# Optimization experiments

Measured on AMD Instinct MI355X. Metric: run time of the kernel, lower is better.

## Reference

```python
import jax, jax.numpy as jnp
import numpy as np

GRID = 4
N = GRID * GRID  # 16 nodes
CIN = 16
HID = 64
HEADS = 4
OUT = 256
NEG_SLOPE = 0.2  # PyG GATConv default leaky relu slope
LN_EPS = 1e-5


def _adj_mask():
    # 4-connected grid adjacency + self loops (PyG GATConv add_self_loops=True)
    m = np.zeros((N, N), dtype=bool)
    for i in range(GRID):
        for j in range(GRID):
            u = i * GRID + j
            if j + 1 < GRID:
                v = i * GRID + j + 1
                m[u, v] = m[v, u] = True
            if i + 1 < GRID:
                v = (i + 1) * GRID + j
                m[u, v] = m[v, u] = True
    np.fill_diagonal(m, True)
    return m

ADJ = jnp.asarray(_adj_mask())  # [N, N], adj[i, j] = j is a (self-)neighbor of i


def gat_layer(h, W, a_src, a_dst, b, concat):
    """PyG GATConv on the fixed grid graph, dense-masked form.
    h: [B, N, Fin]; W: [Fin, HEADS*C]; a_src/a_dst: [HEADS, C]."""
    B = h.shape[0]
    H, C = a_src.shape
    wh = (h @ W).reshape(B, N, H, C)                       # [B, N, H, C]
    e_src = jnp.einsum('bnhc,hc->bnh', wh, a_src)          # alpha_src . Wh_j
    e_dst = jnp.einsum('bnhc,hc->bnh', wh, a_dst)          # alpha_dst . Wh_i
    # score[b, i, j, h]: target i attends to source j
    e = e_dst[:, :, None, :] + e_src[:, None, :, :]
    e = jax.nn.leaky_relu(e, NEG_SLOPE)
    e = jnp.where(ADJ[None, :, :, None], e, -1e9)
    alpha = jax.nn.softmax(e, axis=2)                      # softmax over sources j
    out = jnp.einsum('bijh,bjhc->bihc', alpha, wh)         # [B, N, H, C]
    if concat:
        out = out.reshape(B, N, H * C)
    else:
        out = out.mean(axis=2)
    return out + b


def setup_inputs() -> dict:
    key = jax.random.key(0)
    ks = jax.random.split(key, 24)
    s = 0.05
    B = 16384
    inp = {
        'x': jax.random.normal(ks[0], (B, CIN, GRID, GRID), dtype=jnp.float32),
        'w_in': jax.random.normal(ks[1], (CIN, HID), dtype=jnp.float32) * s,
        'b_in': jnp.zeros((HID,), jnp.float32),
        # GAT layer 0: in 64 -> 4 heads x 64, concat
        'W0': jax.random.normal(ks[2], (HID, HEADS * HID), dtype=jnp.float32) * s,
        'asrc0': jax.random.normal(ks[3], (HEADS, HID), dtype=jnp.float32) * s,
        'adst0': jax.random.normal(ks[4], (HEADS, HID), dtype=jnp.float32) * s,
        'bb0': jnp.zeros((HEADS * HID,), jnp.float32),
        # GAT layer 1: in 256 -> 4 heads x 64, concat
        'W1': jax.random.normal(ks[5], (HEADS * HID, HEADS * HID), dtype=jnp.float32) * s,
        'asrc1': jax.random.normal(ks[6], (HEADS, HID), dtype=jnp.float32) * s,
        'adst1': jax.random.normal(ks[7], (HEADS, HID), dtype=jnp.float32) * s,
        'bb1': jnp.zeros((HEADS * HID,), jnp.float32),
        # GAT layer 2: in 256 -> 4 heads x 64, mean over heads (concat=False)
        'W2': jax.random.normal(ks[8], (HEADS * HID, HEADS * HID), dtype=jnp.float32) * s,
        'asrc2': jax.random.normal(ks[9], (HEADS, HID), dtype=jnp.float32) * s,
        'adst2': jax.random.normal(ks[10], (HEADS, HID), dtype=jnp.float32) * s,
        'bb2': jnp.zeros((HID,), jnp.float32),
        # output MLP: 64 -> 128 (LN, ReLU) -> 256
        'w1': jax.random.normal(ks[11], (HID, OUT // 2), dtype=jnp.float32) * s,
        'b1': jnp.zeros((OUT // 2,), jnp.float32),
        'ln_g': jnp.ones((OUT // 2,), jnp.float32),
        'ln_b': jnp.zeros((OUT // 2,), jnp.float32),
        'w2': jax.random.normal(ks[12], (OUT // 2, OUT), dtype=jnp.float32) * s,
        'b2': jnp.zeros((OUT,), jnp.float32),
    }
    return inp


def reference(x, w_in, b_in, W0, asrc0, adst0, bb0, W1, asrc1, adst1, bb1,
              W2, asrc2, adst2, bb2, w1, b1, ln_g, ln_b, w2, b2):
    B = x.shape[0]
    # grid_to_graph: (B, C, H, W) -> (B, N, C) node features
    h = jnp.transpose(x, (0, 2, 3, 1)).reshape(B, N, CIN)
    h = jax.nn.relu(h @ w_in + b_in)
    h = gat_layer(h, W0, asrc0, adst0, bb0, concat=True)
    h = jax.nn.relu(h)  # dropout is identity at inference
    h = gat_layer(h, W1, asrc1, adst1, bb1, concat=True)
    h = jax.nn.relu(h)
    h = gat_layer(h, W2, asrc2, adst2, bb2, concat=False)  # [B, N, 64]
    g = h.mean(axis=1)  # global_mean_pool over the 16 nodes of each graph
    # MLP with LayerNorm
    y = g @ w1 + b1
    mu = y.mean(axis=-1, keepdims=True)
    var = ((y - mu) ** 2).mean(axis=-1, keepdims=True)
    y = (y - mu) * jax.lax.rsqrt(var + LN_EPS) * ln_g + ln_b
    y = jax.nn.relu(y)
    return y @ w2 + b2
```

## Files before the change

### kernel.cpp

```cpp
#include <hip/hip_runtime.h>
#include <hip/hip_bf16.h>

typedef short s8v __attribute__((ext_vector_type(8)));
typedef short s4v __attribute__((ext_vector_type(4)));
typedef float f4v __attribute__((ext_vector_type(4)));

#define HSTR 264
#define WSTR 36
#define AP   18

__device__ constexpr unsigned KMASK[16] = {
  0x0013u,0x0027u,0x004Eu,0x008Cu,
  0x0131u,0x0272u,0x04E4u,0x08C8u,
  0x1310u,0x2720u,0x4E40u,0x8C80u,
  0x3100u,0x7200u,0xE400u,0xC800u};

__device__ __forceinline__ short f2b(float x){
  __hip_bfloat16 h = __float2bfloat16(x);
  return *reinterpret_cast<short*>(&h);
}
__device__ __forceinline__ float b2f(short s){
  __hip_bfloat16 h = *reinterpret_cast<__hip_bfloat16*>(&s);
  return __bfloat162float(h);
}

__global__ __launch_bounds__(256) void prep_all(
  const float* __restrict__ W0, const float* __restrict__ as0, const float* __restrict__ ad0,
  const float* __restrict__ W1, const float* __restrict__ as1, const float* __restrict__ ad1,
  const float* __restrict__ W2, const float* __restrict__ as2, const float* __restrict__ ad2,
  const float* __restrict__ w_in,
  short* __restrict__ ws)
{
  short* WPin = ws;
  short* WP0  = ws + 2048;
  short* WP1  = ws + 2048 + 17408;
  short* WP2  = ws + 2048 + 17408 + 69632;

  const int t = threadIdx.x, l = t & 63;
  const int gid = blockIdx.x*4 + (t >> 6);

  if (gid < 288){
    const float* W; short* WP; int u = gid, f, s, KS;
    if (u < 32)      { W = W0; WP = WP0; KS = 2; f = u >> 1; s = u & 1; }
    else if (u < 160){ u -= 32;  W = W1; WP = WP1; KS = 8; f = u >> 3; s = u & 7; }
    else             { u -= 160; W = W2; WP = WP2; KS = 8; f = u >> 3; s = u & 7; }
    const int lq = l & 15, quad = l >> 4;
    union { s8v v; short s16[8]; } o;
    #pragma unroll
    for (int j = 0; j < 8; ++j)
      o.s16[j] = f2b(W[(s*32 + quad*8 + j)*256 + f*16 + lq]);
    *(s8v*)(WP + ((f*KS + s)*64 + l)*8) = o.v;
  } else if (gid < 292){
    const int f = gid - 288;
    const int lq = l & 15, quad = l >> 4;
    union { s8v v; short s16[8]; } o;
    #pragma unroll
    for (int j = 0; j < 8; ++j){
      const int k = quad*8 + j;
      o.s16[j] = (k < 16) ? f2b(w_in[k*64 + f*16 + lq]) : (short)0;
    }
    *(s8v*)(WPin + (f*64 + l)*8) = o.v;
  } else {
    int u = gid - 292;
    const float* W; const float* as; const float* ad; short* WP; int KS, k;
    if (u < 64)      { W=W0; as=as0; ad=ad0; WP=WP0; KS=2; k=u; }
    else if (u < 320){ u-=64;  W=W1; as=as1; ad=ad1; WP=WP1; KS=8; k=u; }
    else             { u-=320; W=W2; as=as2; ad=ad2; WP=WP2; KS=8; k=u; }
    float v[8];
    #pragma unroll
    for (int h = 0; h < 4; ++h){
      const float wv_ = W[k*256 + h*64 + l];
      v[h]   = wv_ * as[h*64 + l];
      v[4+h] = wv_ * ad[h*64 + l];
    }
    #pragma unroll
    for (int s = 1; s < 64; s <<= 1)
      #pragma unroll
      for (int uu = 0; uu < 8; ++uu) v[uu] += __shfl_xor(v[uu], s, 64);
    if (l < 16){
      const float r = (l < 8) ? v[l] : 0.f;
      WP[((16*KS + (k >> 5))*64 + ((k >> 3) & 3)*16 + l)*8 + (k & 7)] = f2b(r);
    }
  }
}

template<int KS, bool MEAN>
__device__ __forceinline__ void gat_layer(short* bufH, short* whT, short* alphaS,
    const short* __restrict__ WP, const float* __restrict__ bbias,
    float* gsm, const int t)
{
  const int l = t & 63, wv = t >> 6, lq = l & 15, quad = l >> 4;
  {
    f4v acc[5][2];
    #pragma unroll
    for (int fi = 0; fi < 5; ++fi)
      #pragma unroll
      for (int nt = 0; nt < 2; ++nt) acc[fi][nt] = (f4v){0.f,0.f,0.f,0.f};
    #pragma unroll 2
    for (int s = 0; s < KS; ++s){
      const s8v a0 = *(const s8v*)&bufH[lq*HSTR + s*32 + quad*8];
      const s8v a1 = *(const s8v*)&bufH[(16+lq)*HSTR + s*32 + quad*8];
      #pragma unroll
      for (int fi = 0; fi < 5; ++fi){
        if (fi == 4 && wv != 3) break;
        const int f = (fi == 4) ? 16 : fi*4 + wv;
        const s8v bF = *(const s8v*)&WP[((f*KS + s)*64 + l)*8];
        acc[fi][0] = __builtin_amdgcn_mfma_f32_16x16x32_bf16(a0, bF, acc[fi][0], 0,0,0);
        acc[fi][1] = __builtin_amdgcn_mfma_f32_16x16x32_bf16(a1, bF, acc[fi][1], 0,0,0);
      }
    }
    #pragma unroll
    for (int fi = 0; fi < 5; ++fi){
      if (fi == 4 && (wv != 3 || lq >= 8)) break;
      const int f = (fi == 4) ? 16 : fi*4 + wv;
      #pragma unroll
      for (int nt = 0; nt < 2; ++nt){
        short4 p;
        p.x = f2b(acc[fi][nt][0]); p.y = f2b(acc[fi][nt][1]);
        p.z = f2b(acc[fi][nt][2]); p.w = f2b(acc[fi][nt][3]);
        *(short4*)&whT[(f*16 + lq)*WSTR + nt*16 + quad*4] = p;
      }
    }
  }
  __syncthreads();
  if (t < 128){
    const int g = t >> 6, h = (t >> 4) & 3, i = t & 15;
    const float ed = b2f(whT[(260 + h)*WSTR + g*16 + i]);
    float ev[16];
    #pragma unroll
    for (int c = 0; c < 4; ++c){
      const s4v v = *(const s4v*)&whT[(256 + h)*WSTR + g*16 + c*4];
      ev[c*4+0]=b2f(v[0]); ev[c*4+1]=b2f(v[1]); ev[c*4+2]=b2f(v[2]); ev[c*4+3]=b2f(v[3]);
    }
    const unsigned m = KMASK[i];
    float mx = -1e30f;
    #pragma unroll
    for (int j = 0; j < 16; ++j){
      float e = ed + ev[j];
      e = (e > 0.f) ? e : 0.2f*e;
      ev[j] = e;
      if ((m >> j) & 1u) mx = fmaxf(mx, e);
    }
    float ssum = 0.f;
    #pragma unroll
    for (int j = 0; j < 16; ++j){
      const float a = ((m >> j) & 1u) ? __expf(ev[j] - mx) : 0.f;
      ev[j] = a; ssum += a;
    }
    const float inv = 1.f / ssum;
    unsigned* row = (unsigned*)&alphaS[((g*4 + h)*16 + i)*AP];
    #pragma unroll
    for (int c = 0; c < 8; ++c){
      const unsigned lo = (unsigned)(unsigned short)f2b(ev[2*c]*inv);
      const unsigned hi = (unsigned)(unsigned short)f2b(ev[2*c+1]*inv);
      row[c] = lo | (hi << 16);
    }
  }
  __syncthreads();
  if constexpr (!MEAN){
    const int h = wv;
    union { s8v v; unsigned u[4]; } B[2];
    #pragma unroll
    for (int g = 0; g < 2; ++g){
      const unsigned* ar = (const unsigned*)&alphaS[((g*4 + h)*16 + lq)*AP + (quad & 1)*8];
      const bool act = ((quad >> 1) == g);
      #pragma unroll
      for (int c = 0; c < 4; ++c) B[g].u[c] = act ? ar[c] : 0u;
    }
    #pragma unroll
    for (int ct = 0; ct < 4; ++ct){
      const s8v a = *(const s8v*)&whT[(h*64 + ct*16 + lq)*WSTR + quad*8];
      #pragma unroll
      for (int g = 0; g < 2; ++g){
        f4v d = (f4v){0.f,0.f,0.f,0.f};
        d = __builtin_amdgcn_mfma_f32_16x16x32_bf16(a, B[g].v, d, 0,0,0);
        const int f0 = h*64 + ct*16 + quad*4;
        const float4 bb = *(const float4*)&bbias[f0];
        short4 p;
        p.x = f2b(fmaxf(d[0] + bb.x, 0.f)); p.y = f2b(fmaxf(d[1] + bb.y, 0.f));
        p.z = f2b(fmaxf(d[2] + bb.z, 0.f)); p.w = f2b(fmaxf(d[3] + bb.w, 0.f));
        *(short4*)&bufH[(g*16 + lq)*HSTR + f0] = p;
      }
    }
  } else {
    const int g = wv >> 1;
    union { s8v v; unsigned u[4]; } B[4];
    #pragma unroll
    for (int h = 0; h < 4; ++h){
      const unsigned* ar = (const unsigned*)&alphaS[((g*4 + h)*16 + lq)*AP + (quad & 1)*8];
      const bool act = ((quad >> 1) == g);
      #pragma unroll
      for (int c = 0; c < 4; ++c) B[h].u[c] = act ? ar[c] : 0u;
    }
    #pragma unroll
    for (int cc = 0; cc < 2; ++cc){
      const int ct = (wv & 1)*2 + cc;
      f4v d = (f4v){0.f,0.f,0.f,0.f};
      #pragma unroll
      for (int h = 0; h < 4; ++h){
        const s8v a = *(const s8v*)&whT[(h*64 + ct*16 + lq)*WSTR + quad*8];
        d = __builtin_amdgcn_mfma_f32_16x16x32_bf16(a, B[h].v, d, 0,0,0);
      }
      #pragma unroll
      for (int s = 1; s < 16; s <<= 1){
        d[0] += __shfl_xor(d[0], s, 64); d[1] += __shfl_xor(d[1], s, 64);
        d[2] += __shfl_xor(d[2], s, 64); d[3] += __shfl_xor(d[3], s, 64);
      }
      if (lq == 0){
        const int f0 = ct*16 + quad*4;
        const float4 bb = *(const float4*)&bbias[f0];
        float4 gv;
        gv.x = d[0]*(1.f/64.f) + bb.x; gv.y = d[1]*(1.f/64.f) + bb.y;
        gv.z = d[2]*(1.f/64.f) + bb.z; gv.w = d[3]*(1.f/64.f) + bb.w;
        *(float4*)&gsm[g*64 + f0] = gv;
      }
    }
  }
}

__global__ __launch_bounds__(256, 4) void gat_main(
  const float* __restrict__ x,
  const short* __restrict__ WPin, const float* __restrict__ b_in,
  const short* __restrict__ WP0,  const float* __restrict__ bb0,
  const short* __restrict__ WP1,  const float* __restrict__ bb1,
  const short* __restrict__ WP2,  const float* __restrict__ bb2,
  const float* __restrict__ w1,   const float* __restrict__ b1,
  const float* __restrict__ lng,  const float* __restrict__ lnb,
  const float* __restrict__ w2,   const float* __restrict__ b2,
  float* __restrict__ out)
{
  __shared__ __align__(16) short smem[32*HSTR + 264*WSTR + 8*16*AP];
  short* bufH   = smem;
  short* whT    = smem + 32*HSTR;
  short* alphaS = smem + 32*HSTR + 264*WSTR;
  short* h0   = whT;
  float* gsm  = (float*)bufH;
  float* ylds = gsm + 128;
  float* red  = ylds + 256;
  constexpr int H0S = 40;

  const int b = blockIdx.x;
  const int t = threadIdx.x;
  const int l = t & 63, wv = t >> 6, lq = l & 15, quad = l >> 4;

  {
    const float2 v = *(const float2*)&x[b*512 + 2*t];
    const int i0 = 2*t;
    const int g = i0 >> 8, c = (i0 >> 4) & 15, n = i0 & 15;
    h0[(g*16 + n)*H0S + c]     = f2b(v.x);
    h0[(g*16 + n + 1)*H0S + c] = f2b(v.y);
    const int r = t >> 3, cc = 16 + 2*(t & 7);
    h0[r*H0S + cc] = 0; h0[r*H0S + cc + 1] = 0;
  }
  __syncthreads();

  {
    const s8v aF  = *(const s8v*)&WPin[(wv*64 + l)*8];
    const s8v b0v = *(const s8v*)&h0[lq*H0S + quad*8];
    const s8v b1v = *(const s8v*)&h0[(16+lq)*H0S + quad*8];
    f4v acc0 = (f4v){0.f,0.f,0.f,0.f}, acc1 = (f4v){0.f,0.f,0.f,0.f};
    acc0 = __builtin_amdgcn_mfma_f32_16x16x32_bf16(aF, b0v, acc0, 0,0,0);
    acc1 = __builtin_amdgcn_mfma_f32_16x16x32_bf16(aF, b1v, acc1, 0,0,0);
    const int f0 = wv*16 + quad*4;
    const float4 bi = *(const float4*)&b_in[f0];
    short4 p0, p1;
    p0.x = f2b(fmaxf(acc0[0]+bi.x,0.f)); p0.y = f2b(fmaxf(acc0[1]+bi.y,0.f));
    p0.z = f2b(fmaxf(acc0[2]+bi.z,0.f)); p0.w = f2b(fmaxf(acc0[3]+bi.w,0.f));
    p1.x = f2b(fmaxf(acc1[0]+bi.x,0.f)); p1.y = f2b(fmaxf(acc1[1]+bi.y,0.f));
    p1.z = f2b(fmaxf(acc1[2]+bi.z,0.f)); p1.w = f2b(fmaxf(acc1[3]+bi.w,0.f));
    *(short4*)&bufH[lq*HSTR + f0]      = p0;
    *(short4*)&bufH[(16+lq)*HSTR + f0] = p1;
  }
  __syncthreads();

  gat_layer<2, false>(bufH, whT, alphaS, WP0, bb0, gsm, t);
  __syncthreads();
  gat_layer<8, false>(bufH, whT, alphaS, WP1, bb1, gsm, t);
  __syncthreads();
  gat_layer<8, true >(bufH, whT, alphaS, WP2, bb2, gsm, t);
  __syncthreads();

  const int gg = t >> 7, o = t & 127;
  float yv = b1[o];
  #pragma unroll 8
  for (int k = 0; k < 64; ++k) yv += gsm[gg*64 + k] * w1[k*128 + o];
  float s1 = yv, s2 = yv*yv;
  #pragma unroll
  for (int s = 1; s < 64; s <<= 1){ s1 += __shfl_xor(s1, s, 64); s2 += __shfl_xor(s2, s, 64); }
  if ((t & 63) == 0){ red[(t>>6)*2] = s1; red[(t>>6)*2 + 1] = s2; }
  __syncthreads();
  {
    const float S1 = red[4*gg] + red[4*gg+2], S2 = red[4*gg+1] + red[4*gg+3];
    const float mu  = S1 * (1.f/128.f);
    const float var = S2 * (1.f/128.f) - mu*mu;
    const float yn  = (yv - mu) * rsqrtf(var + 1e-5f) * lng[o] + lnb[o];
    ylds[gg*128 + o] = fmaxf(yn, 0.f);
  }
  __syncthreads();
  float a0 = b2[t], a1 = b2[t];
  #pragma unroll 4
  for (int k = 0; k < 128; ++k){
    const float wv2 = w2[k*256 + t];
    a0 += ylds[k]*wv2; a1 += ylds[128 + k]*wv2;
  }
  out[(b*2 + 0)*256 + t] = a0;
  out[(b*2 + 1)*256 + t] = a1;
}

extern "C" void kernel_launch(void* const* d_in, const int* in_sizes, int n_in,
                              void* d_out, int out_size, void* d_ws, size_t ws_size,
                              hipStream_t stream){
  const float* x    = (const float*)d_in[0];
  const float* w_in = (const float*)d_in[1];
  const float* b_in = (const float*)d_in[2];
  const float* W0   = (const float*)d_in[3];
  const float* as0  = (const float*)d_in[4];
  const float* ad0  = (const float*)d_in[5];
  const float* bb0  = (const float*)d_in[6];
  const float* W1   = (const float*)d_in[7];
  const float* as1  = (const float*)d_in[8];
  const float* ad1  = (const float*)d_in[9];
  const float* bb1  = (const float*)d_in[10];
  const float* W2   = (const float*)d_in[11];
  const float* as2  = (const float*)d_in[12];
  const float* ad2  = (const float*)d_in[13];
  const float* bb2  = (const float*)d_in[14];
  const float* w1   = (const float*)d_in[15];
  const float* b1   = (const float*)d_in[16];
  const float* lng  = (const float*)d_in[17];
  const float* lnb  = (const float*)d_in[18];
  const float* w2   = (const float*)d_in[19];
  const float* b2   = (const float*)d_in[20];
  const int B = in_sizes[0] / 256;

  short* ws = (short*)d_ws;
  const short* WPin = ws;
  const short* WP0  = ws + 2048;
  const short* WP1  = ws + 2048 + 17408;
  const short* WP2  = ws + 2048 + 17408 + 69632;

  prep_all<<<217, 256, 0, stream>>>(W0, as0, ad0, W1, as1, ad1, W2, as2, ad2,
                                    w_in, ws);
  gat_main<<<B/2, 256, 0, stream>>>(x, WPin, b_in, WP0, bb0, WP1, bb1, WP2, bb2,
                                    w1, b1, lng, lnb, w2, b2, (float*)d_out);
}
```

Before: 336.0 us.

## Swizzle node-feature LDS layout, pack bf16 with perm, drop softmax max pass

Reorganizes the node-feature buffer in LDS into a k-slice/quad-blocked layout, so each lane's 8-element MFMA operand load is contiguous and free of bank conflicts, and removes the padded stride. It adds a fast bf16 pair-packing helper built on a rounding add and byte permute, fully unrolls the K loop, hoists the bias load, and drops the max-subtraction pass in the masked softmax. Skipping the max subtraction assumes the attention scores stay small enough that exp does not overflow. The new bf16 rounding ignores NaN handling. AP padding also changes.

Result: no change. 330.2 us (-1.7%).

```diff
diff --git a/kernel.cpp b/kernel.cpp
--- a/kernel.cpp
+++ b/kernel.cpp
@@ -5,9 +5,10 @@
 typedef short s4v __attribute__((ext_vector_type(4)));
 typedef float f4v __attribute__((ext_vector_type(4)));
 
-#define HSTR 264
 #define WSTR 36
-#define AP   18
+#define AP   20
+
+#define HIXBASE(s, quad) (((s)*4 + (quad))*256)
 
 __device__ constexpr unsigned KMASK[16] = {
   0x0013u,0x0027u,0x004Eu,0x008Cu,
@@ -22,6 +23,12 @@
 __device__ __forceinline__ float b2f(short s){
   __hip_bfloat16 h = *reinterpret_cast<__hip_bfloat16*>(&s);
   return __bfloat162float(h);
+}
+__device__ __forceinline__ unsigned pk2(float a, float b){
+  unsigned ua = __float_as_uint(a), ub = __float_as_uint(b);
+  ua += 0x7fffu + ((ua >> 16) & 1u);
+  ub += 0x7fffu + ((ub >> 16) & 1u);
+  return __builtin_amdgcn_perm(ub, ua, 0x07060302);
 }
 
 __global__ __launch_bounds__(256) void prep_all(
@@ -96,10 +103,10 @@
     for (int fi = 0; fi < 5; ++fi)
       #pragma unroll
       for (int nt = 0; nt < 2; ++nt) acc[fi][nt] = (f4v){0.f,0.f,0.f,0.f};
-    #pragma unroll 2
+    #pragma unroll
     for (int s = 0; s < KS; ++s){
-      const s8v a0 = *(const s8v*)&bufH[lq*HSTR + s*32 + quad*8];
-      const s8v a1 = *(const s8v*)&bufH[(16+lq)*HSTR + s*32 + quad*8];
+      const s8v a0 = *(const s8v*)&bufH[HIXBASE(s, quad) + lq*8];
+      const s8v a1 = *(const s8v*)&bufH[HIXBASE(s, quad) + (16 + lq)*8];
       #pragma unroll
       for (int fi = 0; fi < 5; ++fi){
         if (fi == 4 && wv != 3) break;
@@ -115,10 +122,10 @@
       const int f = (fi == 4) ? 16 : fi*4 + wv;
       #pragma unroll
       for (int nt = 0; nt < 2; ++nt){
-        short4 p;
-        p.x = f2b(acc[fi][nt][0]); p.y = f2b(acc[fi][nt][1]);
-        p.z = f2b(acc[fi][nt][2]); p.w = f2b(acc[fi][nt][3]);
-        *(short4*)&whT[(f*16 + lq)*WSTR + nt*16 + quad*4] = p;
+        uint2 p;
+        p.x = pk2(acc[fi][nt][0], acc[fi][nt][1]);
+        p.y = pk2(acc[fi][nt][2], acc[fi][nt][3]);
+        *(uint2*)&whT[(f*16 + lq)*WSTR + nt*16 + quad*4] = p;
       }
     }
   }
@@ -133,28 +140,19 @@
       ev[c*4+0]=b2f(v[0]); ev[c*4+1]=b2f(v[1]); ev[c*4+2]=b2f(v[2]); ev[c*4+3]=b2f(v[3]);
     }
     const unsigned m = KMASK[i];
-    float mx = -1e30f;
+    float ssum = 0.f;
     #pragma unroll
     for (int j = 0; j < 16; ++j){
       float e = ed + ev[j];
       e = (e > 0.f) ? e : 0.2f*e;
-      ev[j] = e;
-      if ((m >> j) & 1u) mx = fmaxf(mx, e);
-    }
-    float ssum = 0.f;
-    #pragma unroll
-    for (int j = 0; j < 16; ++j){
-      const float a = ((m >> j) & 1u) ? __expf(ev[j] - mx) : 0.f;
+      const float a = ((m >> j) & 1u) ? __expf(e) : 0.f;
       ev[j] = a; ssum += a;
     }
     const float inv = 1.f / ssum;
     unsigned* row = (unsigned*)&alphaS[((g*4 + h)*16 + i)*AP];
     #pragma unroll
-    for (int c = 0; c < 8; ++c){
-      const unsigned lo = (unsigned)(unsigned short)f2b(ev[2*c]*inv);
-      const unsigned hi = (unsigned)(unsigned short)f2b(ev[2*c+1]*inv);
-      row[c] = lo | (hi << 16);
-    }
+    for (int c = 0; c < 8; ++c)
+      row[c] = pk2(ev[2*c]*inv, ev[2*c+1]*inv);
   }
   __syncthreads();
   if constexpr (!MEAN){
@@ -170,16 +168,19 @@
     #pragma unroll
     for (int ct = 0; ct < 4; ++ct){
       const s8v a = *(const s8v*)&whT[(h*64 + ct*16 + lq)*WSTR + quad*8];
+      const int sf = h*2 + (ct >> 1);
+      const int qf = (ct & 1)*2 + (quad >> 1);
+      const int jf = (quad & 1)*4;
+      const int f0 = h*64 + ct*16 + quad*4;
+      const float4 bb = *(const float4*)&bbias[f0];
       #pragma unroll
       for (int g = 0; g < 2; ++g){
         f4v d = (f4v){0.f,0.f,0.f,0.f};
         d = __builtin_amdgcn_mfma_f32_16x16x32_bf16(a, B[g].v, d, 0,0,0);
-        const int f0 = h*64 + ct*16 + quad*4;
-        const float4 bb = *(const float4*)&bbias[f0];
-        short4 p;
-        p.x = f2b(fmaxf(d[0] + bb.x, 0.f)); p.y = f2b(fmaxf(d[1] + bb.y, 0.f));
-        p.z = f2b(fmaxf(d[2] + bb.z, 0.f)); p.w = f2b(fmaxf(d[3] + bb.w, 0.f));
-        *(short4*)&bufH[(g*16 + lq)*HSTR + f0] = p;
+        uint2 p;
+        p.x = pk2(fmaxf(d[0] + bb.x, 0.f), fmaxf(d[1] + bb.y, 0.f));
+        p.y = pk2(fmaxf(d[2] + bb.z, 0.f), fmaxf(d[3] + bb.w, 0.f));
+        *(uint2*)&bufH[HIXBASE(sf, qf) + (g*16 + lq)*8 + jf] = p;
       }
     }
   } else {
@@ -229,10 +230,10 @@
   const float* __restrict__ w2,   const float* __restrict__ b2,
   float* __restrict__ out)
 {
-  __shared__ __align__(16) short smem[32*HSTR + 264*WSTR + 8*16*AP];
+  __shared__ __align__(16) short smem[8*4*32*8 + 264*WSTR + 8*16*AP];
   short* bufH   = smem;
-  short* whT    = smem + 32*HSTR;
-  short* alphaS = smem + 32*HSTR + 264*WSTR;
+  short* whT    = smem + 8192;
+  short* alphaS = smem + 8192 + 264*WSTR;
   short* h0   = whT;
   float* gsm  = (float*)bufH;
   float* ylds = gsm + 128;
@@ -263,13 +264,16 @@
     acc1 = __builtin_amdgcn_mfma_f32_16x16x32_bf16(aF, b1v, acc1, 0,0,0);
     const int f0 = wv*16 + quad*4;
     const float4 bi = *(const float4*)&b_in[f0];
-    short4 p0, p1;
-    p0.x = f2b(fmaxf(acc0[0]+bi.x,0.f)); p0.y = f2b(fmaxf(acc0[1]+bi.y,0.f));
-    p0.z = f2b(fmaxf(acc0[2]+bi.z,0.f)); p0.w = f2b(fmaxf(acc0[3]+bi.w,0.f));
-    p1.x = f2b(fmaxf(acc1[0]+bi.x,0.f)); p1.y = f2b(fmaxf(acc1[1]+bi.y,0.f));
-    p1.z = f2b(fmaxf(acc1[2]+bi.z,0.f)); p1.w = f2b(fmaxf(acc1[3]+bi.w,0.f));
-    *(short4*)&bufH[lq*HSTR + f0]      = p0;
-    *(short4*)&bufH[(16+lq)*HSTR + f0] = p1;
+    const int sf = wv >> 1;
+    const int qf = (wv & 1)*2 + (quad >> 1);
+    const int jf = (quad & 1)*4;
+    uint2 p0, p1;
+    p0.x = pk2(fmaxf(acc0[0]+bi.x,0.f), fmaxf(acc0[1]+bi.y,0.f));
+    p0.y = pk2(fmaxf(acc0[2]+bi.z,0.f), fmaxf(acc0[3]+bi.w,0.f));
+    p1.x = pk2(fmaxf(acc1[0]+bi.x,0.f), fmaxf(acc1[1]+bi.y,0.f));
+    p1.y = pk2(fmaxf(acc1[2]+bi.z,0.f), fmaxf(acc1[3]+bi.w,0.f));
+    *(uint2*)&bufH[HIXBASE(sf, qf) + lq*8 + jf]        = p0;
+    *(uint2*)&bufH[HIXBASE(sf, qf) + (16 + lq)*8 + jf] = p1;
   }
   __syncthreads();
 
```
